# Kernel tuning notes

Hardware: AMD Instinct MI355X
Metric: run time of the kernel (lower is better)

## Reference

```python
import jax, jax.numpy as jnp
import numpy as np

B, D, C, K = 8192, 2048, 4096, 1000  # batch, input_dim, num_centers, num_classes


def setup_inputs() -> dict:
    key = jax.random.key(0)
    k0, k1, k2 = jax.random.split(key, 3)
    x = jax.random.normal(k0, (B, D), dtype=jnp.float32)
    centers = jax.random.normal(k1, (C, D), dtype=jnp.float32)
    beta = jnp.ones((C,), dtype=jnp.float32)
    W = jax.random.normal(k2, (K, C), dtype=jnp.float32) * 0.02  # fc.weight
    b = jnp.zeros((K,), dtype=jnp.float32)  # fc.bias
    return {"x": x, "centers": centers, "beta": beta, "W": W, "b": b}


def reference(x, centers, beta, W, b):
    # Pairwise Euclidean distance via the Gram trick (same math as
    # torch.norm(x[:,None,:] - centers, dim=2), without the (B,C,D) intermediate).
    x2 = jnp.sum(x * x, axis=-1, keepdims=True)          # (B, 1)
    c2 = jnp.sum(centers * centers, axis=-1)             # (C,)
    sq = x2 + c2[None, :] - 2.0 * (x @ centers.T)        # (B, C) squared distances
    dist = jnp.sqrt(jnp.maximum(sq, 0.0))
    act = jnp.exp(-beta[None, :] * dist)                 # RBF activations
    act = act / jnp.sum(act, axis=1, keepdims=True)      # normalize over centers
    return act @ W.T + b                                 # linear head (B, K)
```

## Files before the change

### kernel.cpp

```cpp
#include <hip/hip_runtime.h>


#define BB 8192
#define DD 2048
#define CC 4096
#define KK 1000
#define KP 1024

typedef unsigned short u16;
typedef __bf16 bf16x8 __attribute__((ext_vector_type(8)));
typedef float f32x4 __attribute__((ext_vector_type(4)));

typedef const void __attribute__((address_space(1)))* gvp_t;
typedef void __attribute__((address_space(3)))* lvp_t;

__device__ __forceinline__ u16 f2bf(float f) {
  union { float f; unsigned u; } v; v.f = f;
  return (u16)((v.u + 0x7fffu + ((v.u >> 16) & 1u)) >> 16);
}

__global__ void prep_all(const float* __restrict__ x, const float* __restrict__ cen,
                         const float* __restrict__ W,
                         u16* __restrict__ xb, u16* __restrict__ cb,
                         u16* __restrict__ wb,
                         float* __restrict__ x2, float* __restrict__ c2) {
  int row = blockIdx.x;
  int t = threadIdx.x;
  if (row >= BB + CC) {
    int r = row - BB - CC;
    ushort4* dst = reinterpret_cast<ushort4*>(wb + (size_t)r * CC);
    if (r < KK) {
      const float4* src = reinterpret_cast<const float4*>(W + (size_t)r * CC);
#pragma unroll
      for (int m = 0; m < 4; ++m) {
        float4 v = src[t + 256 * m];
        dst[t + 256 * m] = make_ushort4(f2bf(v.x), f2bf(v.y), f2bf(v.z), f2bf(v.w));
      }
    } else {
#pragma unroll
      for (int m = 0; m < 4; ++m) dst[t + 256 * m] = make_ushort4(0, 0, 0, 0);
    }
    return;
  }
  const float* src;
  u16* dst;
  float* nrm;
  if (row < BB) {
    src = x + (size_t)row * DD; dst = xb + (size_t)row * DD; nrm = x2 + row;
  } else {
    int r = row - BB;
    src = cen + (size_t)r * DD; dst = cb + (size_t)r * DD; nrm = c2 + r;
  }
  float s = 0.f;
#pragma unroll
  for (int m = 0; m < 2; ++m) {
    int idx = t + 256 * m;
    float4 v = reinterpret_cast<const float4*>(src)[idx];
    s += v.x * v.x + v.y * v.y + v.z * v.z + v.w * v.w;
    reinterpret_cast<ushort4*>(dst)[idx] =
        make_ushort4(f2bf(v.x), f2bf(v.y), f2bf(v.z), f2bf(v.w));
  }
#pragma unroll
  for (int off = 1; off < 64; off <<= 1) s += __shfl_xor(s, off);
  __shared__ float red[4];
  if ((t & 63) == 0) red[t >> 6] = s;
  __syncthreads();
  if (t == 0) *nrm = red[0] + red[1] + red[2] + red[3];
}

#define SB0 __builtin_amdgcn_sched_barrier(0)
#define BARR __builtin_amdgcn_s_barrier()
#define LGKM0 asm volatile("s_waitcnt lgkmcnt(0)" ::: "memory")


#define ST_A(BUF, H, TILE)                                                         \
  {                                                                                \
    const u16* _s = gA0 + (size_t)((H) * 128) * DD + (TILE) * 64;                  \
    char* _d = (char*)smem + (BUF) * 65536 + (H) * 16384 + t * 16;                 \
    __builtin_amdgcn_global_load_lds((gvp_t)_s, (lvp_t)_d, 16, 0, 0);              \
    __builtin_amdgcn_global_load_lds((gvp_t)(_s + (size_t)64 * DD),                \
                                     (lvp_t)(_d + 8192), 16, 0, 0);                \
  }

#define ST_B(BUF, H, TILE)                                                         \
  {                                                                                \
    const u16* _s = gB0 + (size_t)((H) * 128) * DD + (TILE) * 64;                  \
    char* _d = (char*)smem + (BUF) * 65536 + 32768 + (H) * 16384 + t * 16;         \
    __builtin_amdgcn_global_load_lds((gvp_t)_s, (lvp_t)_d, 16, 0, 0);              \
    __builtin_amdgcn_global_load_lds((gvp_t)(_s + (size_t)64 * DD),                \
                                     (lvp_t)(_d + 8192), 16, 0, 0);                \
  }

#define READ_B(SBP)                                                                \
  _Pragma("unroll") for (int n_ = 0; n_ < 4; ++n_) {                               \
    _Pragma("unroll") for (int ks_ = 0; ks_ < 2; ++ks_) {                          \
      bfr[n_][ks_] = *(const bf16x8*)((SBP) + bRow + n_ * 2048 + cbv[ks_]);        \
    }                                                                              \
  }

#define READ_A(SAP, MQ)                                                            \
  _Pragma("unroll") for (int m_ = 0; m_ < 2; ++m_) {                               \
    _Pragma("unroll") for (int ks_ = 0; ks_ < 2; ++ks_) {                          \
      af[m_][ks_] =                                                                \
          *(const bf16x8*)((SAP) + aRow + ((MQ)*2 + m_) * 2048 + cbv[ks_]);        \
    }                                                                              \
  }

#define MFMA_Q(MQ)                                                                 \
  __builtin_amdgcn_s_setprio(1);                                                   \
  _Pragma("unroll") for (int m_ = 0; m_ < 2; ++m_) {                               \
    _Pragma("unroll") for (int n_ = 0; n_ < 4; ++n_) {                             \
      _Pragma("unroll") for (int ks_ = 0; ks_ < 2; ++ks_) {                        \
        acc[(MQ)*2 + m_][n_] = __builtin_amdgcn_mfma_f32_16x16x32_bf16(            \
            af[m_][ks_], bfr[n_][ks_], acc[(MQ)*2 + m_][n_], 0, 0, 0);             \
      }                                                                            \
    }                                                                              \
  }                                                                                \
  __builtin_amdgcn_s_setprio(0)

#define TILE_BODY(TILE, CUR, DOA, DOB, VMN)                                        \
  {                                                                                \
    const char* sA_ = (const char*)smem + (CUR) * 65536;                           \
    const char* sB_ = sA_ + 32768;                                                 \
    READ_B(sB_);                                                                   \
    READ_A(sA_, 0);                                                               \
    SB0;                                                                           \
    if (DOA) { ST_A(1 - (CUR), 0, (TILE) + 1); ST_A(1 - (CUR), 1, (TILE) + 1); }   \
    SB0; BARR; LGKM0; SB0;                                                         \
    MFMA_Q(0); SB0; BARR;                                                          \
    READ_A(sA_, 1); SB0;                                                           \
    if (DOB) { ST_B((CUR), 0, (TILE) + 2); }                                       \
    SB0; BARR; LGKM0; SB0;                                                         \
    MFMA_Q(1); SB0; BARR;                                                          \
    READ_A(sA_, 2); SB0;                                                           \
    if (DOB) { ST_B((CUR), 1, (TILE) + 2); }                                       \
    SB0; BARR; LGKM0; SB0;                                                         \
    MFMA_Q(2); SB0; BARR;                                                          \
    READ_A(sA_, 3); SB0; BARR; LGKM0; SB0;                                         \
    MFMA_Q(3);                                                                     \
    if ((VMN) == 4) { asm volatile("s_waitcnt vmcnt(4)" ::: "memory"); }           \
    else if ((VMN) == 0) { asm volatile("s_waitcnt vmcnt(0)" ::: "memory"); }      \
    SB0; BARR;                                                                     \
  }

__global__ __launch_bounds__(512, 2)
void gemm1_rbf(const u16* __restrict__ Abf, const u16* __restrict__ Bbf,
               const float* __restrict__ x2, const float* __restrict__ c2,
               const float* __restrict__ beta, u16* __restrict__ Ebf,
               float* __restrict__ psum) {
  constexpr int NT = DD / 64;
  __shared__ __align__(16) char smem[131072];

  const int t = threadIdx.x;
  const int lane = t & 63;
  const int wave = t >> 6;
  const int wr = wave >> 2;
  const int wc = wave & 3;
  const int l15 = lane & 15;

  const int rowBase = blockIdx.y * 256;
  const int colBase = blockIdx.x * 256;

  f32x4 acc[8][4];
#pragma unroll
  for (int i = 0; i < 8; ++i)
#pragma unroll
    for (int j = 0; j < 4; ++j) acc[i][j] = 0.f;

  const int srow = t >> 3;
  const u16* gA0 = Abf + (size_t)(rowBase + srow) * DD + ((t & 7) ^ (srow & 7)) * 8;
  const u16* gB0 = Bbf + (size_t)(colBase + srow) * DD + ((t & 7) ^ (srow & 7)) * 8;

  int cbv[2];
  cbv[0] = (((lane >> 4) & 3) ^ (lane & 7)) << 4;
  cbv[1] = ((4 + ((lane >> 4) & 3)) ^ (lane & 7)) << 4;
  const int aRow = (wr * 128 + l15) * 128;
  const int bRow = (wc * 64 + l15) * 128;

  bf16x8 bfr[4][2];
  bf16x8 af[2][2];

  ST_A(0, 0, 0); ST_A(0, 1, 0); ST_B(0, 0, 0); ST_B(0, 1, 0);
  ST_B(1, 0, 1); ST_B(1, 1, 1);
  asm volatile("s_waitcnt vmcnt(4)" ::: "memory");
  BARR;

#pragma unroll 2
  for (int tile = 0; tile < NT - 2; ++tile) {
    TILE_BODY(tile, tile & 1, true, true, 4);
  }
  TILE_BODY(NT - 2, (NT - 2) & 1, true, false, 0);
  TILE_BODY(NT - 1, (NT - 1) & 1, false, false, -1);

  const int khi4 = (lane >> 4) * 4;
  const int pslot = (blockIdx.x << 2) + wc;
  float c2v[4], bet[4];
  int gc[4];
#pragma unroll
  for (int n = 0; n < 4; ++n) {
    gc[n] = colBase + wc * 64 + n * 16 + l15;
    c2v[n] = c2[gc[n]];
    bet[n] = beta[gc[n]];
  }
#pragma unroll
  for (int m = 0; m < 8; ++m) {
#pragma unroll
    for (int r = 0; r < 4; ++r) {
      const int grow = rowBase + wr * 128 + m * 16 + khi4 + r;
      const float x2v = x2[grow];
      u16* orow = Ebf + (size_t)grow * CC;
      float rs = 0.f;
#pragma unroll
      for (int n = 0; n < 4; ++n) {
        float d = acc[m][n][r];
        float sq = fmaxf(x2v + c2v[n] - 2.0f * d, 0.0f);
        float e = __expf(-bet[n] * __builtin_amdgcn_sqrtf(sq));
        rs += e;
        orow[gc[n]] = f2bf(e);
      }
#pragma unroll
      for (int off = 1; off < 16; off <<= 1) rs += __shfl_xor(rs, off);
      if (l15 == 0) psum[(size_t)grow * 64 + pslot] = rs;
    }
  }
}

__global__ void rowsum_reduce(const float* __restrict__ psum, float* __restrict__ rowsum) {
  const int row = blockIdx.x * 256 + threadIdx.x;
  const float4* p = reinterpret_cast<const float4*>(psum + (size_t)row * 64);
  float s = 0.f;
#pragma unroll
  for (int i = 0; i < 16; ++i) {
    float4 v = p[i];
    s += v.x + v.y + v.z + v.w;
  }
  rowsum[row] = s;
}


#define ST2_A(BUF, H, TILE)                                                        \
  {                                                                                \
    const u16* _s = gA0 + (size_t)((H) * 128) * CC + (TILE) * 64;                  \
    char* _d = (char*)smem + (BUF) * 49152 + (H) * 16384 + t * 16;                 \
    __builtin_amdgcn_global_load_lds((gvp_t)_s, (lvp_t)_d, 16, 0, 0);              \
    __builtin_amdgcn_global_load_lds((gvp_t)(_s + (size_t)64 * CC),                \
                                     (lvp_t)(_d + 8192), 16, 0, 0);                \
  }

#define ST2_B(BUF, TILE)                                                           \
  {                                                                                \
    const u16* _s = gB0 + (TILE) * 64;                                             \
    char* _d = (char*)smem + (BUF) * 49152 + 32768 + t * 16;                       \
    __builtin_amdgcn_global_load_lds((gvp_t)_s, (lvp_t)_d, 16, 0, 0);              \
    __builtin_amdgcn_global_load_lds((gvp_t)(_s + (size_t)64 * CC),                \
                                     (lvp_t)(_d + 8192), 16, 0, 0);                \
  }

#define READ2_B(SBP)                                                               \
  _Pragma("unroll") for (int n_ = 0; n_ < 2; ++n_) {                               \
    _Pragma("unroll") for (int ks_ = 0; ks_ < 2; ++ks_) {                          \
      bfr[n_][ks_] = *(const bf16x8*)((SBP) + bRow + n_ * 2048 + cbv[ks_]);        \
    }                                                                              \
  }

#define READ2_A(SAP, MQ)                                                           \
  _Pragma("unroll") for (int m_ = 0; m_ < 2; ++m_) {                               \
    _Pragma("unroll") for (int ks_ = 0; ks_ < 2; ++ks_) {                          \
      af[m_][ks_] =                                                                \
          *(const bf16x8*)((SAP) + aRow + ((MQ)*2 + m_) * 2048 + cbv[ks_]);        \
    }                                                                              \
  }

#define MFMA2_Q(MQ)                                                                \
  __builtin_amdgcn_s_setprio(1);                                                   \
  _Pragma("unroll") for (int m_ = 0; m_ < 2; ++m_) {                               \
    _Pragma("unroll") for (int n_ = 0; n_ < 2; ++n_) {                             \
      _Pragma("unroll") for (int ks_ = 0; ks_ < 2; ++ks_) {                        \
        acc[(MQ)*2 + m_][n_] = __builtin_amdgcn_mfma_f32_16x16x32_bf16(            \
            af[m_][ks_], bfr[n_][ks_], acc[(MQ)*2 + m_][n_], 0, 0, 0);             \
      }                                                                            \
    }                                                                              \
  }                                                                                \
  __builtin_amdgcn_s_setprio(0)

#define TILE2_BODY(TILE, CUR, DOA, DOB, VMN)                                       \
  {                                                                                \
    const char* sA_ = (const char*)smem + (CUR) * 49152;                           \
    const char* sB_ = sA_ + 32768;                                                 \
    READ2_B(sB_);                                                                  \
    READ2_A(sA_, 0);                                                               \
    SB0;                                                                           \
    if (DOA) { ST2_A(1 - (CUR), 0, (TILE) + 1); }                                  \
    SB0; BARR; LGKM0; SB0;                                                         \
    MFMA2_Q(0); SB0; BARR;                                                         \
    READ2_A(sA_, 1); SB0;                                                          \
    if (DOA) { ST2_A(1 - (CUR), 1, (TILE) + 1); }                                  \
    SB0; BARR; LGKM0; SB0;                                                         \
    MFMA2_Q(1); SB0; BARR;                                                         \
    READ2_A(sA_, 2); SB0;                                                          \
    if (DOB) { ST2_B((CUR), (TILE) + 2); }                                         \
    SB0; BARR; LGKM0; SB0;                                                         \
    MFMA2_Q(2); SB0; BARR;                                                         \
    READ2_A(sA_, 3); SB0; BARR; LGKM0; SB0;                                        \
    MFMA2_Q(3);                                                                    \
    if ((VMN) == 2) { asm volatile("s_waitcnt vmcnt(2)" ::: "memory"); }           \
    else if ((VMN) == 0) { asm volatile("s_waitcnt vmcnt(0)" ::: "memory"); }      \
    SB0; BARR;                                                                     \
  }

__global__ __launch_bounds__(512, 2)
void gemm2_out(const u16* __restrict__ Ebf, const u16* __restrict__ Wbf,
               const float* __restrict__ rowsum, const float* __restrict__ bias,
               float* __restrict__ out) {
  constexpr int NT = CC / 64;
  __shared__ __align__(16) char smem[98304];

  const int t = threadIdx.x;
  const int lane = t & 63;
  const int wave = t >> 6;
  const int wr = wave >> 2;
  const int wc = wave & 3;
  const int l15 = lane & 15;

  const int d = blockIdx.x + (blockIdx.y << 3);
  const int s_ = d >> 3;
  const int by = (d & 7) + ((s_ >> 3) << 3);
  const int bx = s_ & 7;

  const int rowBase = by * 256;
  const int colBase = bx * 128;

  f32x4 acc[8][2];
#pragma unroll
  for (int i = 0; i < 8; ++i)
#pragma unroll
    for (int j = 0; j < 2; ++j) acc[i][j] = 0.f;

  const int srow = t >> 3;
  const u16* gA0 = Ebf + (size_t)(rowBase + srow) * CC + ((t & 7) ^ (srow & 7)) * 8;
  const u16* gB0 = Wbf + (size_t)(colBase + srow) * CC + ((t & 7) ^ (srow & 7)) * 8;

  int cbv[2];
  cbv[0] = (((lane >> 4) & 3) ^ (lane & 7)) << 4;
  cbv[1] = ((4 + ((lane >> 4) & 3)) ^ (lane & 7)) << 4;
  const int aRow = (wr * 128 + l15) * 128;
  const int bRow = (wc * 32 + l15) * 128;

  bf16x8 bfr[2][2];
  bf16x8 af[2][2];

  ST2_A(0, 0, 0); ST2_A(0, 1, 0); ST2_B(0, 0);
  ST2_B(1, 1);
  asm volatile("s_waitcnt vmcnt(2)" ::: "memory");
  BARR;

#pragma unroll 2
  for (int tile = 0; tile < NT - 2; ++tile) {
    TILE2_BODY(tile, tile & 1, true, true, 2);
  }
  TILE2_BODY(NT - 2, (NT - 2) & 1, true, false, 0);
  TILE2_BODY(NT - 1, (NT - 1) & 1, false, false, -1);

  const int khi4 = (lane >> 4) * 4;
  int gc[2];
  float bv[2];
#pragma unroll
  for (int n = 0; n < 2; ++n) {
    gc[n] = colBase + wc * 32 + n * 16 + l15;
    bv[n] = (gc[n] < KK) ? bias[gc[n]] : 0.f;
  }
#pragma unroll
  for (int m = 0; m < 8; ++m) {
#pragma unroll
    for (int r = 0; r < 4; ++r) {
      const int grow = rowBase + wr * 128 + m * 16 + khi4 + r;
      const float inv = 1.0f / rowsum[grow];
#pragma unroll
      for (int n = 0; n < 2; ++n) {
        if (gc[n] < KK)
          out[(size_t)grow * KK + gc[n]] = acc[m][n][r] * inv + bv[n];
      }
    }
  }
}

#define OFF_XB 0u
#define OFF_CB 33554432u
#define OFF_WB 50331648u
#define OFF_EB 58720256u
#define OFF_X2 125829120u
#define OFF_C2 125861888u
#define OFF_RS 125878272u

extern "C" void kernel_launch(void* const* d_in, const int* in_sizes, int n_in,
                              void* d_out, int out_size, void* d_ws, size_t ws_size,
                              hipStream_t stream) {
  const float* x = (const float*)d_in[0];
  const float* cen = (const float*)d_in[1];
  const float* beta = (const float*)d_in[2];
  const float* W = (const float*)d_in[3];
  const float* bias = (const float*)d_in[4];
  float* out = (float*)d_out;
  char* ws = (char*)d_ws;

  u16* xb = (u16*)(ws + OFF_XB);
  u16* cb = (u16*)(ws + OFF_CB);
  u16* wb = (u16*)(ws + OFF_WB);
  u16* eb = (u16*)(ws + OFF_EB);
  float* x2 = (float*)(ws + OFF_X2);
  float* c2 = (float*)(ws + OFF_C2);
  float* rowsum = (float*)(ws + OFF_RS);
  float* psum = out;

  prep_all<<<BB + CC + KP, 256, 0, stream>>>(x, cen, W, xb, cb, wb, x2, c2);
  gemm1_rbf<<<dim3(CC / 256, BB / 256), 512, 0, stream>>>(xb, cb, x2, c2, beta, eb, psum);
  rowsum_reduce<<<BB / 256, 256, 0, stream>>>(psum, rowsum);
  gemm2_out<<<dim3(KP / 128, BB / 256), 512, 0, stream>>>(eb, wb, rowsum, bias, out);
}
```

Before: 345.7 us.

## Drop redundant intra-tile barriers and reduce row sums through LDS

Removes most of the workgroup barriers inside the two GEMM tile bodies, keeping only those needed around buffer reuse, to cut synchronization stalls between MFMA quarters. It also replaces the per-row cross-lane shuffle reduction and strided partial-sum writes in the RBF epilogue with an LDS staging buffer. A single pass then sums each row and writes one partial per block in a column-major layout, which the reduce kernel reads coalesced. Removing barriers risks races if any waves still read LDS regions that the async global-to-LDS loads overwrite.

```diff
diff --git a/kernel.cpp b/kernel.cpp
--- a/kernel.cpp
+++ b/kernel.cpp
@@ -123,20 +123,20 @@
     const char* sA_ = (const char*)smem + (CUR) * 65536;                           \
     const char* sB_ = sA_ + 32768;                                                 \
     READ_B(sB_);                                                                   \
-    READ_A(sA_, 0);                                                               \
+    READ_A(sA_, 0);                                                                \
     SB0;                                                                           \
     if (DOA) { ST_A(1 - (CUR), 0, (TILE) + 1); ST_A(1 - (CUR), 1, (TILE) + 1); }   \
-    SB0; BARR; LGKM0; SB0;                                                         \
+    SB0; LGKM0; SB0;                                                               \
     MFMA_Q(0); SB0; BARR;                                                          \
     READ_A(sA_, 1); SB0;                                                           \
     if (DOB) { ST_B((CUR), 0, (TILE) + 2); }                                       \
-    SB0; BARR; LGKM0; SB0;                                                         \
-    MFMA_Q(1); SB0; BARR;                                                          \
+    SB0; LGKM0; SB0;                                                               \
+    MFMA_Q(1); SB0;                                                                \
     READ_A(sA_, 2); SB0;                                                           \
     if (DOB) { ST_B((CUR), 1, (TILE) + 2); }                                       \
-    SB0; BARR; LGKM0; SB0;                                                         \
-    MFMA_Q(2); SB0; BARR;                                                          \
-    READ_A(sA_, 3); SB0; BARR; LGKM0; SB0;                                         \
+    SB0; LGKM0; SB0;                                                               \
+    MFMA_Q(2); SB0;                                                                \
+    READ_A(sA_, 3); SB0; LGKM0; SB0;                                               \
     MFMA_Q(3);                                                                     \
     if ((VMN) == 4) { asm volatile("s_waitcnt vmcnt(4)" ::: "memory"); }           \
     else if ((VMN) == 0) { asm volatile("s_waitcnt vmcnt(0)" ::: "memory"); }      \
@@ -193,7 +193,7 @@
   TILE_BODY(NT - 1, (NT - 1) & 1, false, false, -1);
 
   const int khi4 = (lane >> 4) * 4;
-  const int pslot = (blockIdx.x << 2) + wc;
+  float* lrs = (float*)smem;
   float c2v[4], bet[4];
   int gc[4];
 #pragma unroll
@@ -206,7 +206,8 @@
   for (int m = 0; m < 8; ++m) {
 #pragma unroll
     for (int r = 0; r < 4; ++r) {
-      const int grow = rowBase + wr * 128 + m * 16 + khi4 + r;
+      const int rrel = wr * 128 + m * 16 + khi4 + r;
+      const int grow = rowBase + rrel;
       const float x2v = x2[grow];
       u16* orow = Ebf + (size_t)grow * CC;
       float rs = 0.f;
@@ -218,22 +219,27 @@
         rs += e;
         orow[gc[n]] = f2bf(e);
       }
-#pragma unroll
-      for (int off = 1; off < 16; off <<= 1) rs += __shfl_xor(rs, off);
-      if (l15 == 0) psum[(size_t)grow * 64 + pslot] = rs;
+      lrs[rrel * 68 + wc * 16 + l15] = rs;
     }
+  }
+  __syncthreads();
+  if (t < 256) {
+    const f32x4* p = (const f32x4*)(lrs + t * 68);
+    float s = 0.f;
+#pragma unroll
+    for (int i = 0; i < 16; ++i) {
+      f32x4 v = p[i];
+      s += v[0] + v[1] + v[2] + v[3];
+    }
+    psum[(size_t)blockIdx.x * BB + rowBase + t] = s;
   }
 }
 
 __global__ void rowsum_reduce(const float* __restrict__ psum, float* __restrict__ rowsum) {
   const int row = blockIdx.x * 256 + threadIdx.x;
-  const float4* p = reinterpret_cast<const float4*>(psum + (size_t)row * 64);
   float s = 0.f;
 #pragma unroll
-  for (int i = 0; i < 16; ++i) {
-    float4 v = p[i];
-    s += v.x + v.y + v.z + v.w;
-  }
+  for (int b = 0; b < 16; ++b) s += psum[(size_t)b * BB + row];
   rowsum[row] = s;
 }
 
@@ -291,17 +297,17 @@
     READ2_A(sA_, 0);                                                               \
     SB0;                                                                           \
     if (DOA) { ST2_A(1 - (CUR), 0, (TILE) + 1); }                                  \
-    SB0; BARR; LGKM0; SB0;                                                         \
+    SB0; LGKM0; SB0;                                                               \
     MFMA2_Q(0); SB0; BARR;                                                         \
     READ2_A(sA_, 1); SB0;                                                          \
     if (DOA) { ST2_A(1 - (CUR), 1, (TILE) + 1); }                                  \
-    SB0; BARR; LGKM0; SB0;                                                         \
-    MFMA2_Q(1); SB0; BARR;                                                         \
+    SB0; LGKM0; SB0;                                                               \
+    MFMA2_Q(1); SB0;                                                               \
     READ2_A(sA_, 2); SB0;                                                          \
     if (DOB) { ST2_B((CUR), (TILE) + 2); }                                         \
-    SB0; BARR; LGKM0; SB0;                                                         \
-    MFMA2_Q(2); SB0; BARR;                                                         \
-    READ2_A(sA_, 3); SB0; BARR; LGKM0; SB0;                                        \
+    SB0; LGKM0; SB0;                                                               \
+    MFMA2_Q(2); SB0;                                                               \
+    READ2_A(sA_, 3); SB0; LGKM0; SB0;                                              \
     MFMA2_Q(3);                                                                    \
     if ((VMN) == 2) { asm volatile("s_waitcnt vmcnt(2)" ::: "memory"); }           \
     else if ((VMN) == 0) { asm volatile("s_waitcnt vmcnt(0)" ::: "memory"); }      \
```

Result: faster. 337.6 us (-2.3%).
